# Kernel tuning notes

Measured on AMD Instinct MI355X. Metric: run time of the kernel, lower is better.

## Reference

```python
import jax, jax.numpy as jnp
import numpy as np

E = 16      # num_experts
K = 4       # num_experts_per_tok
H = 2048    # hidden_size
I = 1408    # moe_intermediate_size
SI = 5632   # shared expert intermediate size
CAP = 1024
NORM_TOPK = False


def setup_inputs() -> dict:
    key = jax.random.key(0)
    ks = jax.random.split(key, 9)
    def w(k, shape, fan_in):
        return jax.random.normal(k, shape, jnp.float32) * (fan_in ** -0.5)
    return {
        "hidden_states": jax.random.normal(ks[0], (1, 2048, H), jnp.float32),
        "gate_w":  w(ks[1], (E, H), H),        # router: Linear(H -> E), no bias
        "we_gate": w(ks[2], (E, I, H), H),     # per-expert gate_proj weights
        "we_up":   w(ks[3], (E, I, H), H),     # per-expert up_proj weights
        "we_down": w(ks[4], (E, H, I), I),     # per-expert down_proj weights
        "ws_gate": w(ks[5], (SI, H), H),       # shared expert gate_proj
        "ws_up":   w(ks[6], (SI, H), H),       # shared expert up_proj
        "ws_down": w(ks[7], (H, SI), SI),      # shared expert down_proj
        "sg_w":    w(ks[8], (1, H), H),        # shared_expert_gate: Linear(H -> 1)
    }


def reference(hidden_states, gate_w, we_gate, we_up, we_down,
              ws_gate, ws_up, ws_down, sg_w):
    B, S, Hd = hidden_states.shape
    x = hidden_states.reshape(-1, Hd)                      # [T, H]
    T = x.shape[0]

    # --- router ---
    router_logits = x @ gate_w.T                           # [T, E]
    probs = jax.nn.softmax(router_logits.astype(jnp.float32), axis=-1)
    topw, topi = jax.lax.top_k(probs, K)                   # [T, K]
    if NORM_TOPK:
        topw = topw / topw.sum(axis=-1, keepdims=True)

    # --- dispatch: flatten (token, slot) assignments ---
    A = T * K
    fe = topi.reshape(A)                                   # expert id per assignment
    fw = topw.reshape(A)                                   # routing weight per assignment
    ft = jnp.repeat(jnp.arange(T), K)                      # token id per assignment
    # position of each assignment within its expert (rank in arrival order)
    oh = jax.nn.one_hot(fe, E, dtype=jnp.int32)            # [A, E]
    pos = jnp.take_along_axis(jnp.cumsum(oh, axis=0) - 1, fe[:, None], axis=1)[:, 0]
    valid = pos < CAP
    # scatter tokens into per-expert buffers; overflow goes to dummy row CAP
    buf = jnp.zeros((E, CAP + 1, Hd), x.dtype)
    buf = buf.at[fe, jnp.where(valid, pos, CAP)].set(x[ft])[:, :CAP]  # [E, C, H]

    # --- per-expert SiLU-gated MLP (batched grouped GEMMs) ---
    g = jnp.einsum('ech,eih->eci', buf, we_gate)
    u = jnp.einsum('ech,eih->eci', buf, we_up)
    eo = jnp.einsum('eci,ehi->ech', jax.nn.silu(g) * u, we_down)      # [E, C, H]

    # --- combine: weighted scatter-add back to tokens ---
    ga = eo[fe, jnp.minimum(pos, CAP - 1)]                 # [A, H]
    wcomb = (fw * valid.astype(fw.dtype)).astype(x.dtype)
    y = jnp.zeros((T, Hd), x.dtype).at[ft].add(ga * wcomb[:, None])

    # --- shared expert with sigmoid gate ---
    sh = (jax.nn.silu(x @ ws_gate.T) * (x @ ws_up.T)) @ ws_down.T
    sh = jax.nn.sigmoid(x @ sg_w.T) * sh

    out = (y + sh).reshape(B, S, Hd)
    return out, router_logits
```

## Files before the change

kernel.cpp:

```cpp
#include <hip/hip_runtime.h>

#define T_TOK 2048
#define NE 16
#define KTOP 4
#define HD 2048
#define ID 1408
#define SID 5632
#define CAPACITY 1024

typedef __attribute__((ext_vector_type(8))) short short8;
typedef __attribute__((ext_vector_type(4))) float floatx4;

__device__ __forceinline__ short f2b(float f){
  union { float f; unsigned u; } v; v.f = f;
  unsigned r = v.u + 0x7fffu + ((v.u >> 16) & 1u);
  return (short)(r >> 16);
}
__device__ __forceinline__ float b2f(short s){
  union { float f; unsigned u; } v; v.u = ((unsigned)(unsigned short)s) << 16;
  return v.f;
}
__device__ __forceinline__ unsigned cvt_pk(float a, float b){
  unsigned r;
  asm("v_cvt_pk_bf16_f32 %0, %1, %2" : "=v"(r) : "v"(a), "v"(b));
  return r;
}
__device__ __forceinline__ short8 cvt8(float4 a, float4 b){
  union { unsigned d[4]; short8 s; } u;
  u.d[0] = cvt_pk(a.x, a.y); u.d[1] = cvt_pk(a.z, a.w);
  u.d[2] = cvt_pk(b.x, b.y); u.d[3] = cvt_pk(b.z, b.w);
  return u.s;
}
__device__ __forceinline__ void gl16(const void* g, void* l){
  __builtin_amdgcn_global_load_lds(
      (const __attribute__((address_space(1))) void*)g,
      (__attribute__((address_space(3))) void*)l, 16, 0, 0);
}

__device__ __forceinline__ void conv_range(
    int cb, int ncb,
    const float* __restrict__ s1, short* __restrict__ d1, long long n1,
    const float* __restrict__ s2, short* __restrict__ d2, long long n2)
{
  const long long tot = n1 + n2;
  const long long stride = (long long)ncb * 256;
  #pragma unroll 2
  for (long long i = (long long)cb * 256 + threadIdx.x; i < tot; i += stride){
    const float* s; short8* d; long long j;
    if (i < n1){ s = s1; d = (short8*)d1; j = i; }
    else       { s = s2; d = (short8*)d2; j = i - n1; }
    float4 f0 = ((const float4*)s)[j * 2];
    float4 f1 = ((const float4*)s)[j * 2 + 1];
    d[j] = cvt8(f0, f1);
  }
}
__device__ __forceinline__ void conv3(
    int cb, int ncb,
    const float* __restrict__ s1, short* __restrict__ d1, long long n1,
    const float* __restrict__ s2, short* __restrict__ d2, long long n2,
    const float* __restrict__ s3, short* __restrict__ d3, long long n3)
{
  const long long tot = n1 + n2 + n3;
  const long long stride = (long long)ncb * 256;
  #pragma unroll 2
  for (long long i = (long long)cb * 256 + threadIdx.x; i < tot; i += stride){
    const float* s; short8* d; long long j;
    if (i < n1){ s = s1; d = (short8*)d1; j = i; }
    else if (i < n1 + n2){ s = s2; d = (short8*)d2; j = i - n1; }
    else { s = s3; d = (short8*)d3; j = i - n1 - n2; }
    float4 f0 = ((const float4*)s)[j * 2];
    float4 f1 = ((const float4*)s)[j * 2 + 1];
    d[j] = cvt8(f0, f1);
  }
}

__global__ void moe_router(const float* __restrict__ x,
                           const float* __restrict__ gate_w,
                           const float* __restrict__ sg_w,
                           float* __restrict__ logits_out,
                           short* __restrict__ xb,
                           int* __restrict__ counts,
                           int* __restrict__ slot_token,
                           int* __restrict__ tslot,
                           float* __restrict__ tw,
                           float* __restrict__ sg,
                           const float* cs1, short* cd1, long long cn1,
                           const float* cs2, short* cd2, long long cn2,
                           const float* cs3, short* cd3, long long cn3)
{
  if (blockIdx.x >= 512){
    conv3(blockIdx.x - 512, gridDim.x - 512, cs1, cd1, cn1, cs2, cd2, cn2, cs3, cd3, cn3);
    return;
  }
  int wave = threadIdx.x >> 6, lane = threadIdx.x & 63;
  int t = (blockIdx.x << 2) + wave;
  const float4* xr = (const float4*)(x + (size_t)t * HD);
  short8* xbw = (short8*)(xb + (size_t)t * HD);
  float acc[17];
  #pragma unroll
  for (int e = 0; e < 17; ++e) acc[e] = 0.f;
  #pragma unroll
  for (int j = 0; j < 4; ++j){
    int i4 = (j * 64 + lane) * 2;
    float4 x0 = xr[i4], x1 = xr[i4 + 1];
    xbw[j * 64 + lane] = cvt8(x0, x1);
    #pragma unroll
    for (int e = 0; e < 16; ++e){
      const float4* gr = (const float4*)(gate_w + e * HD);
      float4 g0 = gr[i4], g1 = gr[i4 + 1];
      acc[e] += x0.x*g0.x + x0.y*g0.y + x0.z*g0.z + x0.w*g0.w
              + x1.x*g1.x + x1.y*g1.y + x1.z*g1.z + x1.w*g1.w;
    }
    const float4* sr = (const float4*)sg_w;
    float4 s0 = sr[i4], s1 = sr[i4 + 1];
    acc[16] += x0.x*s0.x + x0.y*s0.y + x0.z*s0.z + x0.w*s0.w
             + x1.x*s1.x + x1.y*s1.y + x1.z*s1.z + x1.w*s1.w;
  }
  #pragma unroll
  for (int e = 0; e < 17; ++e){
    float v = acc[e];
    #pragma unroll
    for (int off = 32; off > 0; off >>= 1) v += __shfl_xor(v, off, 64);
    acc[e] = v;
  }
  if (lane == 0){
    float m = acc[0];
    #pragma unroll
    for (int e = 1; e < 16; ++e) m = fmaxf(m, acc[e]);
    float p[16]; float s = 0.f;
    #pragma unroll
    for (int e = 0; e < 16; ++e){ p[e] = expf(acc[e] - m); s += p[e]; }
    float inv = 1.f / s;
    #pragma unroll
    for (int e = 0; e < 16; ++e) logits_out[t * 16 + e] = acc[e];
    unsigned used = 0;
    for (int k = 0; k < KTOP; ++k){
      float best = -1.f; int bi = 0;
      #pragma unroll
      for (int e = 0; e < 16; ++e){
        float pe = ((used >> e) & 1u) ? -1.f : p[e];
        if (pe > best){ best = pe; bi = e; }
      }
      used |= (1u << bi);
      int pos = atomicAdd(&counts[bi], 1);
      int enc = -1;
      if (pos < CAPACITY){
        slot_token[bi * CAPACITY + pos] = t;
        enc = bi * CAPACITY + pos;
      }
      tslot[t * KTOP + k] = enc;
      tw[t * KTOP + k] = best * inv;
    }
    sg[t] = 1.f / (1.f + expf(-acc[16]));
  }
}


#define GEMM_PREAMBLE \
  const int tid = threadIdx.x; \
  const int lane = tid & 63, wave = tid >> 6; \
  const int wr = wave >> 1, wc = wave & 1; \
  const int lrow = lane & 15, lk = lane >> 4; \
  const int s_th = (tid & 7) ^ ((tid >> 3) & 7); \
  const int koff = (s_th & 3) << 3; \
  const int rloc = ((tid >> 3) << 1) + (s_th >> 2); \
  const int lb = lrow >> 1; \
  const int soff = (((((lrow & 1) << 2) | lk) ^ (lb & 7)) << 4); \
  const int abase = (wr * 32 + lb) * 128 + soff;

#define WAIT8  asm volatile("s_waitcnt vmcnt(8)" ::: "memory");
#define WAIT4  asm volatile("s_waitcnt vmcnt(4)" ::: "memory");
#define WAIT0  asm volatile("s_waitcnt vmcnt(0)" ::: "memory");
#define SBAR   asm volatile("s_barrier" ::: "memory");

__device__ __forceinline__ void dev_gateup(
    char (&smem)[3][16384],
    const short* __restrict__ Asrc,
    const short* __restrict__ Wg, const short* __restrict__ Wu,
    short* __restrict__ Out,
    const int* __restrict__ counts, const int* __restrict__ slot_token,
    int Ndim, int Kdim, int expert_mode, int mtiles, int ntiles,
    int bid, int nwg)
{
  int wg = ((bid & 7) * (nwg >> 3)) + (bid >> 3);
  int m_t = wg % mtiles; wg /= mtiles;
  int n_t = wg % ntiles; int e = wg / ntiles;

  int cnt = T_TOK; size_t woff = 0; short* out = Out;
  if (expert_mode){
    cnt = counts[e]; if (cnt > CAPACITY) cnt = CAPACITY;
    if (m_t * 128 >= cnt) return;
    woff = (size_t)e * Ndim * Kdim;
    out = Out + (size_t)e * CAPACITY * Ndim;
  }
  const int m0 = m_t * 128, n0 = n_t * 64;

  GEMM_PREAMBLE
  const int gbase = 8192 + (wc * 16 + lb) * 128 + soff;

  const short* aP0;
  const short* aP1;
  {
    int p0 = m0 + rloc, p1 = m0 + 64 + rloc;
    if (expert_mode){
      int q0 = (p0 < cnt) ? p0 : 0, q1 = (p1 < cnt) ? p1 : 0;
      aP0 = Asrc + (size_t)slot_token[e * CAPACITY + q0] * Kdim + koff;
      aP1 = Asrc + (size_t)slot_token[e * CAPACITY + q1] * Kdim + koff;
    } else {
      aP0 = Asrc + (size_t)p0 * Kdim + koff;
      aP1 = Asrc + (size_t)p1 * Kdim + koff;
    }
  }
  const short* bgP = Wg + woff + (size_t)(n0 + rloc) * Kdim + koff;
  const short* buP = Wu + woff + (size_t)(n0 + rloc) * Kdim + koff;

  const floatx4 vzero = {0.f, 0.f, 0.f, 0.f};
  floatx4 accg[4][2], accu[4][2];
  #pragma unroll
  for (int i = 0; i < 4; ++i)
    #pragma unroll
    for (int j = 0; j < 2; ++j){ accg[i][j] = vzero; accu[i][j] = vzero; }

#define GU_ISSUE(B, T) { char* _b = (B); const int _k = (T) << 5; \
    gl16(aP0 + _k, _b + tid * 16); \
    gl16(aP1 + _k, _b + 4096 + tid * 16); \
    gl16(bgP + _k, _b + 8192 + tid * 16); \
    gl16(buP + _k, _b + 12288 + tid * 16); }

#define GU_COMPUTE(B) { const char* bb = (B); \
    short8 a[4], bg[2], bu[2]; \
    _Pragma("unroll") \
    for (int mf = 0; mf < 4; ++mf) a[mf] = *(const short8*)(bb + abase + mf * 1024); \
    _Pragma("unroll") \
    for (int nf = 0; nf < 2; ++nf){ \
      bg[nf] = *(const short8*)(bb + gbase + nf * 1024); \
      bu[nf] = *(const short8*)(bb + gbase + 4096 + nf * 1024); } \
    __builtin_amdgcn_s_setprio(1); \
    _Pragma("unroll") \
    for (int mf = 0; mf < 4; ++mf) \
      _Pragma("unroll") \
      for (int nf = 0; nf < 2; ++nf){ \
        accg[mf][nf] = __builtin_amdgcn_mfma_f32_16x16x32_bf16(a[mf], bg[nf], accg[mf][nf], 0, 0, 0); \
        accu[mf][nf] = __builtin_amdgcn_mfma_f32_16x16x32_bf16(a[mf], bu[nf], accu[mf][nf], 0, 0, 0); } \
    __builtin_amdgcn_s_setprio(0); }

  const int NSTEP = Kdim >> 5;
  char* b0 = smem[0];
  char* b1 = smem[1];
  char* b2 = smem[2];
  GU_ISSUE(b0, 0)
  GU_ISSUE(b1, 1)
  for (int s = 0; s < NSTEP; ++s){
    if (s + 2 < NSTEP){ GU_ISSUE(b2, s + 2) WAIT8 }
    else if (s + 2 == NSTEP){ WAIT4 }
    else { WAIT0 }
    SBAR
    GU_COMPUTE(b0)
    SBAR
    char* t = b0; b0 = b1; b1 = b2; b2 = t;
  }

  const int colbase = n0 + wc * 32 + lrow;
  #pragma unroll
  for (int mf = 0; mf < 4; ++mf){
    int pr = m0 + wr * 64 + mf * 16 + lk * 4;
    #pragma unroll
    for (int nf = 0; nf < 2; ++nf){
      floatx4 g4 = accg[mf][nf], u4 = accu[mf][nf];
      int col = colbase + nf * 16;
      #pragma unroll
      for (int r = 0; r < 4; ++r){
        float gv = g4[r], uv = u4[r];
        float a = (gv / (1.f + __expf(-gv))) * uv;
        out[(size_t)(pr + r) * Ndim + col] = f2b(a);
      }
    }
  }
}

__device__ __forceinline__ void dev_down4(
    char (&smem)[3][16384],
    const short* __restrict__ Asrc, const short* __restrict__ Wd,
    float* __restrict__ y, short* __restrict__ eo,
    const int* __restrict__ counts, const int* __restrict__ slot_token,
    const float* __restrict__ sgate,
    int Kdim, int expert_mode, int mtiles, int ntiles, int bid, int nwg)
{
  int wg = ((bid & 7) * (nwg >> 3)) + (bid >> 3);
  int m_t = wg % mtiles; wg /= mtiles;
  int n_t = wg % ntiles; int e = wg / ntiles;

  int cnt = T_TOK; const short* ab = Asrc; size_t woff = 0;
  if (expert_mode){
    cnt = counts[e]; if (cnt > CAPACITY) cnt = CAPACITY;
    if (m_t * 128 >= cnt) return;
    ab = Asrc + (size_t)e * CAPACITY * Kdim;
    woff = (size_t)e * HD * Kdim;
  }
  const int m0 = m_t * 128, n0 = n_t * 128;

  GEMM_PREAMBLE
  const int bbase = 8192 + (wc * 32 + lb) * 128 + soff;

  const short* aP0 = ab + (size_t)(m0 + rloc) * Kdim + koff;
  const short* aP1 = ab + (size_t)(m0 + 64 + rloc) * Kdim + koff;
  const short* bP0 = Wd + woff + (size_t)(n0 + rloc) * Kdim + koff;
  const short* bP1 = Wd + woff + (size_t)(n0 + 64 + rloc) * Kdim + koff;

  const floatx4 vzero = {0.f, 0.f, 0.f, 0.f};
  floatx4 acc[4][4];
  #pragma unroll
  for (int i = 0; i < 4; ++i)
    #pragma unroll
    for (int j = 0; j < 4; ++j) acc[i][j] = vzero;

#define DN_ISSUE(B, T) { char* _b = (B); const int _k = (T) << 5; \
    gl16(aP0 + _k, _b + tid * 16); \
    gl16(aP1 + _k, _b + 4096 + tid * 16); \
    gl16(bP0 + _k, _b + 8192 + tid * 16); \
    gl16(bP1 + _k, _b + 12288 + tid * 16); }

#define DN_COMPUTE(B) { const char* bb = (B); \
    short8 a[4], b[4]; \
    _Pragma("unroll") \
    for (int mf = 0; mf < 4; ++mf) a[mf] = *(const short8*)(bb + abase + mf * 1024); \
    _Pragma("unroll") \
    for (int nf = 0; nf < 4; ++nf) b[nf] = *(const short8*)(bb + bbase + nf * 1024); \
    __builtin_amdgcn_s_setprio(1); \
    _Pragma("unroll") \
    for (int mf = 0; mf < 4; ++mf) \
      _Pragma("unroll") \
      for (int nf = 0; nf < 4; ++nf) \
        acc[mf][nf] = __builtin_amdgcn_mfma_f32_16x16x32_bf16(a[mf], b[nf], acc[mf][nf], 0, 0, 0); \
    __builtin_amdgcn_s_setprio(0); }

  const int NSTEP = Kdim >> 5;
  char* b0 = smem[0];
  char* b1 = smem[1];
  char* b2 = smem[2];
  DN_ISSUE(b0, 0)
  DN_ISSUE(b1, 1)
  for (int s = 0; s < NSTEP; ++s){
    if (s + 2 < NSTEP){ DN_ISSUE(b2, s + 2) WAIT8 }
    else if (s + 2 == NSTEP){ WAIT4 }
    else { WAIT0 }
    SBAR
    DN_COMPUTE(b0)
    SBAR
    char* t = b0; b0 = b1; b1 = b2; b2 = t;
  }

  const int colb = n0 + wc * 64 + lrow;
  if (expert_mode){
    #pragma unroll
    for (int mf = 0; mf < 4; ++mf){
      int pr = m0 + wr * 64 + mf * 16 + lk * 4;
      #pragma unroll
      for (int r = 0; r < 4; ++r){
        int p = pr + r;
        #pragma unroll
        for (int nf = 0; nf < 4; ++nf)
          eo[(size_t)(e * CAPACITY + p) * HD + colb + nf * 16] = f2b(acc[mf][nf][r]);
      }
    }
  } else {
    #pragma unroll
    for (int mf = 0; mf < 4; ++mf){
      int pr = m0 + wr * 64 + mf * 16 + lk * 4;
      #pragma unroll
      for (int r = 0; r < 4; ++r){
        int t = pr + r;
        float sv = sgate[t];
        #pragma unroll
        for (int nf = 0; nf < 4; ++nf)
          y[(size_t)t * HD + colb + nf * 16] = sv * acc[mf][nf][r];
      }
    }
  }
}

__global__ __launch_bounds__(256) void moe_gateup_sh(
    const short* __restrict__ xb,
    const short* __restrict__ wbsg, const short* __restrict__ wbsu,
    short* __restrict__ acts,
    const float* cs1, short* cd1, long long cn1,
    const float* cs2, short* cd2, long long cn2, int conv_nwg)
{
  __shared__ __align__(16) char smem[3][16384];
  if ((int)blockIdx.x < conv_nwg){
    conv_range(blockIdx.x, conv_nwg, cs1, cd1, cn1, cs2, cd2, cn2);
    return;
  }
  dev_gateup(smem, xb, wbsg, wbsu, acts, nullptr, nullptr, SID, HD, 0, 16, 88,
             blockIdx.x - conv_nwg, gridDim.x - conv_nwg);
}

__global__ __launch_bounds__(256) void moe_mid(
    const short* __restrict__ xb,
    const short* __restrict__ wbeg, const short* __restrict__ wbeu,
    short* __restrict__ act,
    const short* __restrict__ acts, const short* __restrict__ wbsd,
    float* __restrict__ y, const float* __restrict__ sg,
    const int* __restrict__ counts, const int* __restrict__ slot_token,
    const float* ed, short* wbed, long long n_ed)
{
  __shared__ __align__(16) char smem[3][16384];
  int bx = blockIdx.x;
  if (bx < 512){
    conv_range(bx, 512, ed, wbed, n_ed, nullptr, nullptr, 0);
    return;
  }
  bx -= 512;
  if (bx < 256){
    dev_down4(smem, acts, wbsd, y, nullptr, nullptr, nullptr, sg,
              SID, 0, 16, 16, bx, 256);
    return;
  }
  bx -= 256;
  dev_gateup(smem, xb, wbeg, wbeu, act, counts, slot_token, ID, HD, 1, 8, 22,
             bx, 2816);
}

__global__ __launch_bounds__(256) void moe_down_ex(
    const short* __restrict__ act, const short* __restrict__ wbed,
    float* __restrict__ y, short* __restrict__ eo,
    const int* __restrict__ counts, const int* __restrict__ slot_token)
{
  __shared__ __align__(16) char smem[3][16384];
  dev_down4(smem, act, wbed, y, eo, counts, slot_token, nullptr,
            ID, 1, 8, 16, blockIdx.x, gridDim.x);
}

__global__ void moe_combine(const short* __restrict__ eo,
                            const int* __restrict__ tslot,
                            const float* __restrict__ tw,
                            float* __restrict__ y)
{
  int t = blockIdx.x;
  int o = threadIdx.x << 3;
  float* yp = y + (size_t)t * HD + o;
  float4 a0 = *(const float4*)yp, a1 = *(const float4*)(yp + 4);
  float acc[8] = {a0.x, a0.y, a0.z, a0.w, a1.x, a1.y, a1.z, a1.w};
  #pragma unroll
  for (int k = 0; k < KTOP; ++k){
    int s = tslot[t * KTOP + k];
    if (s >= 0){
      float w = tw[t * KTOP + k];
      short8 v = *(const short8*)(eo + (size_t)s * HD + o);
      #pragma unroll
      for (int j = 0; j < 8; ++j) acc[j] += w * b2f(v[j]);
    }
  }
  float4 r0 = {acc[0], acc[1], acc[2], acc[3]};
  float4 r1 = {acc[4], acc[5], acc[6], acc[7]};
  *(float4*)yp = r0; *(float4*)(yp + 4) = r1;
}

extern "C" void kernel_launch(void* const* d_in, const int* in_sizes, int n_in,
                              void* d_out, int out_size, void* d_ws, size_t ws_size,
                              hipStream_t stream)
{
  (void)in_sizes; (void)n_in; (void)out_size; (void)ws_size;
  const float* x       = (const float*)d_in[0];
  const float* gate_w  = (const float*)d_in[1];
  const float* we_gate = (const float*)d_in[2];
  const float* we_up   = (const float*)d_in[3];
  const float* we_down = (const float*)d_in[4];
  const float* wsg     = (const float*)d_in[5];
  const float* wsu     = (const float*)d_in[6];
  const float* wsd     = (const float*)d_in[7];
  const float* sg_w    = (const float*)d_in[8];

  float* y      = (float*)d_out;
  float* logits = y + (size_t)T_TOK * HD;

  const size_t N_EW = (size_t)NE * ID * HD;
  const size_t N_SW = (size_t)SID * HD;
  const long long G_EW = (long long)(N_EW / 8);
  const long long G_SW = (long long)(N_SW / 8);

  char* ws = (char*)d_ws;
  size_t off = 0;
  short* xb   = (short*)(ws + off); off += (size_t)T_TOK * HD * 2;
  short* wb   = (short*)(ws + off); off += (3 * N_EW + 3 * N_SW) * 2;
  short* act  = (short*)(ws + off); off += (size_t)NE * CAPACITY * ID * 2;
  short* acts = (short*)(ws + off); off += (size_t)T_TOK * SID * 2;
  int*   slot_token = (int*)  (ws + off); off += 65536;
  int*   tslot      = (int*)  (ws + off); off += 32768;
  float* tw         = (float*)(ws + off); off += 32768;
  int*   counts     = (int*)  (ws + off); off += 256;
  float* sg         = (float*)(ws + off);

  short* wbeg = wb;
  short* wbeu = wb + N_EW;
  short* wbed = wb + 2 * N_EW;
  short* wbsg = wb + 3 * N_EW;
  short* wbsu = wb + 3 * N_EW + N_SW;
  short* wbsd = wb + 3 * N_EW + 2 * N_SW;
  short* eo = wbeg;

  hipMemsetAsync(counts, 0, 64, stream);
  moe_router<<<512 + 1024, 256, 0, stream>>>(x, gate_w, sg_w, logits, xb,
                                             counts, slot_token, tslot, tw, sg,
                                             wsg, wbsg, G_SW, wsu, wbsu, G_SW,
                                             wsd, wbsd, G_SW);
  moe_gateup_sh<<<512 + 16 * 88, 256, 0, stream>>>(xb, wbsg, wbsu, acts,
                                                   we_gate, wbeg, G_EW,
                                                   we_up, wbeu, G_EW, 512);
  moe_mid<<<512 + 256 + 2816, 256, 0, stream>>>(xb, wbeg, wbeu, act,
                                                acts, wbsd, y, sg,
                                                counts, slot_token,
                                                we_down, wbed, G_EW);
  moe_down_ex<<<8 * 16 * NE, 256, 0, stream>>>(act, wbed, y, eo, counts, slot_token);
  moe_combine<<<T_TOK, 256, 0, stream>>>(eo, tslot, tw, y);
}
```

Before: 735.3 us.

## Double N tile width in gate/up and down GEMMs to raise operand reuse

Widens the N tile of the gate/up GEMM from 64 to 128 columns and of the down GEMM from 128 to 256. Shared memory stages grow to 24 KB, accumulators double, and the wait counts and grid sizes change to match. Each loaded A tile is now reused across twice as many output columns, cutting global and LDS traffic per FLOP. In exchange it uses more registers and LDS, which lowers occupancy, and it launches half as many workgroups, which risks underfilling the CUs, especially for the expert GEMMs whose tiles beyond the per-expert count exit early.

```diff
diff --git a/kernel.cpp b/kernel.cpp
--- a/kernel.cpp
+++ b/kernel.cpp
@@ -168,13 +168,13 @@
   const int soff = (((((lrow & 1) << 2) | lk) ^ (lb & 7)) << 4); \
   const int abase = (wr * 32 + lb) * 128 + soff;
 
-#define WAIT8  asm volatile("s_waitcnt vmcnt(8)" ::: "memory");
-#define WAIT4  asm volatile("s_waitcnt vmcnt(4)" ::: "memory");
+#define WAIT12 asm volatile("s_waitcnt vmcnt(12)" ::: "memory");
+#define WAIT6  asm volatile("s_waitcnt vmcnt(6)" ::: "memory");
 #define WAIT0  asm volatile("s_waitcnt vmcnt(0)" ::: "memory");
 #define SBAR   asm volatile("s_barrier" ::: "memory");
 
 __device__ __forceinline__ void dev_gateup(
-    char (&smem)[3][16384],
+    char (&smem)[3][24576],
     const short* __restrict__ Asrc,
     const short* __restrict__ Wg, const short* __restrict__ Wu,
     short* __restrict__ Out,
@@ -193,10 +193,10 @@
     woff = (size_t)e * Ndim * Kdim;
     out = Out + (size_t)e * CAPACITY * Ndim;
   }
-  const int m0 = m_t * 128, n0 = n_t * 64;
+  const int m0 = m_t * 128, n0 = n_t * 128;
 
   GEMM_PREAMBLE
-  const int gbase = 8192 + (wc * 16 + lb) * 128 + soff;
+  const int browb = wc * 4096 + lb * 128 + soff;
 
   const short* aP0;
   const short* aP1;
@@ -211,37 +211,47 @@
       aP1 = Asrc + (size_t)p1 * Kdim + koff;
     }
   }
-  const short* bgP = Wg + woff + (size_t)(n0 + rloc) * Kdim + koff;
-  const short* buP = Wu + woff + (size_t)(n0 + rloc) * Kdim + koff;
+  const short* bgP0 = Wg + woff + (size_t)(n0 + rloc) * Kdim + koff;
+  const short* bgP1 = Wg + woff + (size_t)(n0 + 64 + rloc) * Kdim + koff;
+  const short* buP0 = Wu + woff + (size_t)(n0 + rloc) * Kdim + koff;
+  const short* buP1 = Wu + woff + (size_t)(n0 + 64 + rloc) * Kdim + koff;
 
   const floatx4 vzero = {0.f, 0.f, 0.f, 0.f};
-  floatx4 accg[4][2], accu[4][2];
+  floatx4 accg[4][4], accu[4][4];
   #pragma unroll
   for (int i = 0; i < 4; ++i)
     #pragma unroll
-    for (int j = 0; j < 2; ++j){ accg[i][j] = vzero; accu[i][j] = vzero; }
+    for (int j = 0; j < 4; ++j){ accg[i][j] = vzero; accu[i][j] = vzero; }
 
 #define GU_ISSUE(B, T) { char* _b = (B); const int _k = (T) << 5; \
     gl16(aP0 + _k, _b + tid * 16); \
     gl16(aP1 + _k, _b + 4096 + tid * 16); \
-    gl16(bgP + _k, _b + 8192 + tid * 16); \
-    gl16(buP + _k, _b + 12288 + tid * 16); }
+    gl16(bgP0 + _k, _b + 8192 + tid * 16); \
+    gl16(bgP1 + _k, _b + 12288 + tid * 16); \
+    gl16(buP0 + _k, _b + 16384 + tid * 16); \
+    gl16(buP1 + _k, _b + 20480 + tid * 16); }
 
 #define GU_COMPUTE(B) { const char* bb = (B); \
-    short8 a[4], bg[2], bu[2]; \
+    short8 a[4], bg[4], bu[4]; \
     _Pragma("unroll") \
     for (int mf = 0; mf < 4; ++mf) a[mf] = *(const short8*)(bb + abase + mf * 1024); \
     _Pragma("unroll") \
-    for (int nf = 0; nf < 2; ++nf){ \
-      bg[nf] = *(const short8*)(bb + gbase + nf * 1024); \
-      bu[nf] = *(const short8*)(bb + gbase + 4096 + nf * 1024); } \
+    for (int nf = 0; nf < 4; ++nf) bg[nf] = *(const short8*)(bb + 8192 + browb + nf * 1024); \
     __builtin_amdgcn_s_setprio(1); \
     _Pragma("unroll") \
     for (int mf = 0; mf < 4; ++mf) \
       _Pragma("unroll") \
-      for (int nf = 0; nf < 2; ++nf){ \
+      for (int nf = 0; nf < 4; ++nf) \
         accg[mf][nf] = __builtin_amdgcn_mfma_f32_16x16x32_bf16(a[mf], bg[nf], accg[mf][nf], 0, 0, 0); \
-        accu[mf][nf] = __builtin_amdgcn_mfma_f32_16x16x32_bf16(a[mf], bu[nf], accu[mf][nf], 0, 0, 0); } \
+    __builtin_amdgcn_s_setprio(0); \
+    _Pragma("unroll") \
+    for (int nf = 0; nf < 4; ++nf) bu[nf] = *(const short8*)(bb + 16384 + browb + nf * 1024); \
+    __builtin_amdgcn_s_setprio(1); \
+    _Pragma("unroll") \
+    for (int mf = 0; mf < 4; ++mf) \
+      _Pragma("unroll") \
+      for (int nf = 0; nf < 4; ++nf) \
+        accu[mf][nf] = __builtin_amdgcn_mfma_f32_16x16x32_bf16(a[mf], bu[nf], accu[mf][nf], 0, 0, 0); \
     __builtin_amdgcn_s_setprio(0); }
 
   const int NSTEP = Kdim >> 5;
@@ -251,8 +261,8 @@
   GU_ISSUE(b0, 0)
   GU_ISSUE(b1, 1)
   for (int s = 0; s < NSTEP; ++s){
-    if (s + 2 < NSTEP){ GU_ISSUE(b2, s + 2) WAIT8 }
-    else if (s + 2 == NSTEP){ WAIT4 }
+    if (s + 2 < NSTEP){ GU_ISSUE(b2, s + 2) WAIT12 }
+    else if (s + 2 == NSTEP){ WAIT6 }
     else { WAIT0 }
     SBAR
     GU_COMPUTE(b0)
@@ -260,12 +270,12 @@
     char* t = b0; b0 = b1; b1 = b2; b2 = t;
   }
 
-  const int colbase = n0 + wc * 32 + lrow;
+  const int colbase = n0 + wc * 64 + lrow;
   #pragma unroll
   for (int mf = 0; mf < 4; ++mf){
     int pr = m0 + wr * 64 + mf * 16 + lk * 4;
     #pragma unroll
-    for (int nf = 0; nf < 2; ++nf){
+    for (int nf = 0; nf < 4; ++nf){
       floatx4 g4 = accg[mf][nf], u4 = accu[mf][nf];
       int col = colbase + nf * 16;
       #pragma unroll
@@ -278,8 +288,8 @@
   }
 }
 
-__device__ __forceinline__ void dev_down4(
-    char (&smem)[3][16384],
+__device__ __forceinline__ void dev_down(
+    char (&smem)[3][24576],
     const short* __restrict__ Asrc, const short* __restrict__ Wd,
     float* __restrict__ y, short* __restrict__ eo,
     const int* __restrict__ counts, const int* __restrict__ slot_token,
@@ -297,40 +307,53 @@
     ab = Asrc + (size_t)e * CAPACITY * Kdim;
     woff = (size_t)e * HD * Kdim;
   }
-  const int m0 = m_t * 128, n0 = n_t * 128;
+  const int m0 = m_t * 128, n0 = n_t * 256;
 
   GEMM_PREAMBLE
-  const int bbase = 8192 + (wc * 32 + lb) * 128 + soff;
+  const int bbase = wc * 8192 + lb * 128 + soff;
 
   const short* aP0 = ab + (size_t)(m0 + rloc) * Kdim + koff;
   const short* aP1 = ab + (size_t)(m0 + 64 + rloc) * Kdim + koff;
   const short* bP0 = Wd + woff + (size_t)(n0 + rloc) * Kdim + koff;
   const short* bP1 = Wd + woff + (size_t)(n0 + 64 + rloc) * Kdim + koff;
+  const short* bP2 = Wd + woff + (size_t)(n0 + 128 + rloc) * Kdim + koff;
+  const short* bP3 = Wd + woff + (size_t)(n0 + 192 + rloc) * Kdim + koff;
 
   const floatx4 vzero = {0.f, 0.f, 0.f, 0.f};
-  floatx4 acc[4][4];
+  floatx4 acc[4][8];
   #pragma unroll
   for (int i = 0; i < 4; ++i)
     #pragma unroll
-    for (int j = 0; j < 4; ++j) acc[i][j] = vzero;
+    for (int j = 0; j < 8; ++j) acc[i][j] = vzero;
 
 #define DN_ISSUE(B, T) { char* _b = (B); const int _k = (T) << 5; \
     gl16(aP0 + _k, _b + tid * 16); \
     gl16(aP1 + _k, _b + 4096 + tid * 16); \
     gl16(bP0 + _k, _b + 8192 + tid * 16); \
-    gl16(bP1 + _k, _b + 12288 + tid * 16); }
+    gl16(bP1 + _k, _b + 12288 + tid * 16); \
+    gl16(bP2 + _k, _b + 16384 + tid * 16); \
+    gl16(bP3 + _k, _b + 20480 + tid * 16); }
 
 #define DN_COMPUTE(B) { const char* bb = (B); \
-    short8 a[4], b[4]; \
+    short8 a[4], b[8]; \
     _Pragma("unroll") \
     for (int mf = 0; mf < 4; ++mf) a[mf] = *(const short8*)(bb + abase + mf * 1024); \
     _Pragma("unroll") \
-    for (int nf = 0; nf < 4; ++nf) b[nf] = *(const short8*)(bb + bbase + nf * 1024); \
+    for (int nf = 0; nf < 4; ++nf) b[nf] = *(const short8*)(bb + 8192 + bbase + nf * 1024); \
     __builtin_amdgcn_s_setprio(1); \
     _Pragma("unroll") \
     for (int mf = 0; mf < 4; ++mf) \
       _Pragma("unroll") \
       for (int nf = 0; nf < 4; ++nf) \
+        acc[mf][nf] = __builtin_amdgcn_mfma_f32_16x16x32_bf16(a[mf], b[nf], acc[mf][nf], 0, 0, 0); \
+    __builtin_amdgcn_s_setprio(0); \
+    _Pragma("unroll") \
+    for (int nf = 4; nf < 8; ++nf) b[nf] = *(const short8*)(bb + 8192 + bbase + nf * 1024); \
+    __builtin_amdgcn_s_setprio(1); \
+    _Pragma("unroll") \
+    for (int mf = 0; mf < 4; ++mf) \
+      _Pragma("unroll") \
+      for (int nf = 4; nf < 8; ++nf) \
         acc[mf][nf] = __builtin_amdgcn_mfma_f32_16x16x32_bf16(a[mf], b[nf], acc[mf][nf], 0, 0, 0); \
     __builtin_amdgcn_s_setprio(0); }
 
@@ -341,8 +364,8 @@
   DN_ISSUE(b0, 0)
   DN_ISSUE(b1, 1)
   for (int s = 0; s < NSTEP; ++s){
-    if (s + 2 < NSTEP){ DN_ISSUE(b2, s + 2) WAIT8 }
-    else if (s + 2 == NSTEP){ WAIT4 }
+    if (s + 2 < NSTEP){ DN_ISSUE(b2, s + 2) WAIT12 }
+    else if (s + 2 == NSTEP){ WAIT6 }
     else { WAIT0 }
     SBAR
     DN_COMPUTE(b0)
@@ -350,7 +373,7 @@
     char* t = b0; b0 = b1; b1 = b2; b2 = t;
   }
 
-  const int colb = n0 + wc * 64 + lrow;
+  const int colb = n0 + wc * 128 + lrow;
   if (expert_mode){
     #pragma unroll
     for (int mf = 0; mf < 4; ++mf){
@@ -359,7 +382,7 @@
       for (int r = 0; r < 4; ++r){
         int p = pr + r;
         #pragma unroll
-        for (int nf = 0; nf < 4; ++nf)
+        for (int nf = 0; nf < 8; ++nf)
           eo[(size_t)(e * CAPACITY + p) * HD + colb + nf * 16] = f2b(acc[mf][nf][r]);
       }
     }
@@ -372,7 +395,7 @@
         int t = pr + r;
         float sv = sgate[t];
         #pragma unroll
-        for (int nf = 0; nf < 4; ++nf)
+        for (int nf = 0; nf < 8; ++nf)
           y[(size_t)t * HD + colb + nf * 16] = sv * acc[mf][nf][r];
       }
     }
@@ -386,12 +409,12 @@
     const float* cs1, short* cd1, long long cn1,
     const float* cs2, short* cd2, long long cn2, int conv_nwg)
 {
-  __shared__ __align__(16) char smem[3][16384];
+  __shared__ __align__(16) char smem[3][24576];
   if ((int)blockIdx.x < conv_nwg){
     conv_range(blockIdx.x, conv_nwg, cs1, cd1, cn1, cs2, cd2, cn2);
     return;
   }
-  dev_gateup(smem, xb, wbsg, wbsu, acts, nullptr, nullptr, SID, HD, 0, 16, 88,
+  dev_gateup(smem, xb, wbsg, wbsu, acts, nullptr, nullptr, SID, HD, 0, 16, 44,
              blockIdx.x - conv_nwg, gridDim.x - conv_nwg);
 }
 
@@ -404,21 +427,21 @@
     const int* __restrict__ counts, const int* __restrict__ slot_token,
     const float* ed, short* wbed, long long n_ed)
 {
-  __shared__ __align__(16) char smem[3][16384];
+  __shared__ __align__(16) char smem[3][24576];
   int bx = blockIdx.x;
   if (bx < 512){
     conv_range(bx, 512, ed, wbed, n_ed, nullptr, nullptr, 0);
     return;
   }
   bx -= 512;
-  if (bx < 256){
-    dev_down4(smem, acts, wbsd, y, nullptr, nullptr, nullptr, sg,
-              SID, 0, 16, 16, bx, 256);
+  if (bx < 128){
+    dev_down(smem, acts, wbsd, y, nullptr, nullptr, nullptr, sg,
+             SID, 0, 16, 8, bx, 128);
     return;
   }
-  bx -= 256;
-  dev_gateup(smem, xb, wbeg, wbeu, act, counts, slot_token, ID, HD, 1, 8, 22,
-             bx, 2816);
+  bx -= 128;
+  dev_gateup(smem, xb, wbeg, wbeu, act, counts, slot_token, ID, HD, 1, 8, 11,
+             bx, 1408);
 }
 
 __global__ __launch_bounds__(256) void moe_down_ex(
@@ -426,9 +449,9 @@
     float* __restrict__ y, short* __restrict__ eo,
     const int* __restrict__ counts, const int* __restrict__ slot_token)
 {
-  __shared__ __align__(16) char smem[3][16384];
-  dev_down4(smem, act, wbed, y, eo, counts, slot_token, nullptr,
-            ID, 1, 8, 16, blockIdx.x, gridDim.x);
+  __shared__ __align__(16) char smem[3][24576];
+  dev_down(smem, act, wbed, y, eo, counts, slot_token, nullptr,
+           ID, 1, 8, 8, blockIdx.x, gridDim.x);
 }
 
 __global__ void moe_combine(const short* __restrict__ eo,
@@ -504,13 +527,13 @@
                                              counts, slot_token, tslot, tw, sg,
                                              wsg, wbsg, G_SW, wsu, wbsu, G_SW,
                                              wsd, wbsd, G_SW);
-  moe_gateup_sh<<<512 + 16 * 88, 256, 0, stream>>>(xb, wbsg, wbsu, acts,
+  moe_gateup_sh<<<512 + 16 * 44, 256, 0, stream>>>(xb, wbsg, wbsu, acts,
                                                    we_gate, wbeg, G_EW,
                                                    we_up, wbeu, G_EW, 512);
-  moe_mid<<<512 + 256 + 2816, 256, 0, stream>>>(xb, wbeg, wbeu, act,
-                                                acts, wbsd, y, sg,
-                                                counts, slot_token,
-                                                we_down, wbed, G_EW);
-  moe_down_ex<<<8 * 16 * NE, 256, 0, stream>>>(act, wbed, y, eo, counts, slot_token);
+  moe_mid<<<512 + 128 + 8 * 11 * NE, 256, 0, stream>>>(xb, wbeg, wbeu, act,
+                                                       acts, wbsd, y, sg,
+                                                       counts, slot_token,
+                                                       we_down, wbed, G_EW);
+  moe_down_ex<<<8 * 8 * NE, 256, 0, stream>>>(act, wbed, y, eo, counts, slot_token);
   moe_combine<<<T_TOK, 256, 0, stream>>>(eo, tslot, tw, y);
 }
```

New measurement: 867.0 us. +17.9%, slower.
